# Performance work log

Measured on AMD Instinct MI355X. Metric: run time of the kernel, lower is better.

Reference implementation:

```python
import jax, jax.numpy as jnp
import numpy as np

D_MODEL = 1024
N_HEADS = 16
HEAD_DIM = D_MODEL // N_HEADS
SCALE = HEAD_DIM ** -0.5
MIN_VAL = jnp.finfo(jnp.float32).min


def setup_inputs() -> dict:
    key = jax.random.key(0)
    ks = jax.random.split(key, 7)
    B, T = 1, 2048
    s = D_MODEL ** -0.5
    return {
        "x": jax.random.normal(ks[0], (B, T, D_MODEL), dtype=jnp.float32),
        "Wq": jax.random.normal(ks[1], (D_MODEL, D_MODEL), dtype=jnp.float32) * s,
        "Wk1": jax.random.normal(ks[2], (D_MODEL, D_MODEL), dtype=jnp.float32) * s,
        "Wk2": jax.random.normal(ks[3], (D_MODEL, D_MODEL), dtype=jnp.float32) * s,
        "Wv": jax.random.normal(ks[4], (D_MODEL, D_MODEL), dtype=jnp.float32) * s,
        "Wo": jax.random.normal(ks[5], (D_MODEL, D_MODEL), dtype=jnp.float32) * s,
        "lambda_logit": jnp.zeros((N_HEADS,), dtype=jnp.float32),  # logit(0.5)=0
    }


def _split_heads(y):
    B, T, _ = y.shape
    return y.reshape(B, T, N_HEADS, HEAD_DIM).transpose(0, 2, 1, 3)  # [B,H,T,hd]


def reference(x, Wq, Wk1, Wk2, Wv, Wo, lambda_logit):
    B, T, _ = x.shape
    q = _split_heads(x @ Wq.T)
    k1 = _split_heads(x @ Wk1.T)
    k2 = _split_heads(x @ Wk2.T)
    v = _split_heads(x @ Wv.T)

    s1 = jnp.einsum("bhqd,bhkd->bhqk", q, k1) * SCALE
    s2 = jnp.einsum("bhqd,bhkd->bhqk", q, k2) * SCALE

    causal = jnp.arange(T)[None, :] <= jnp.arange(T)[:, None]  # [T,T] keep mask
    s1 = jnp.where(causal[None, None], s1, MIN_VAL)
    s2 = jnp.where(causal[None, None], s2, MIN_VAL)

    attn_exp = jax.nn.softmax(s1, axis=-1)
    attn_noise = jax.nn.softmax(s2, axis=-1)
    lam = jax.nn.sigmoid(lambda_logit)[None, :, None, None]
    attn = attn_exp - lam * attn_noise
    denom = jnp.maximum(jnp.sum(jnp.abs(attn), axis=-1, keepdims=True), 1e-6)
    attn = attn / denom

    out = jnp.einsum("bhqk,bhkd->bhqd", attn, v)
    out = out.transpose(0, 2, 1, 3).reshape(B, T, D_MODEL)
    return out @ Wo.T
```

## Files before the change

### kernel.cpp

```cpp
#include <hip/hip_runtime.h>

#define T_SEQ 2048
#define DM 1024
#define NH 16
#define HD 64
#define SC2 0.1803368801111731f
#define LS 80

typedef unsigned short u16;
typedef unsigned int u32;
typedef __attribute__((ext_vector_type(8))) short bf16x8;
typedef __attribute__((ext_vector_type(4))) float f32x4;

static __device__ __forceinline__ f32x4 mfma16(bf16x8 a, bf16x8 b, f32x4 c) {
    return __builtin_amdgcn_mfma_f32_16x16x32_bf16(a, b, c, 0, 0, 0);
}
static __device__ __forceinline__ float bf2f(u16 u) {
    union { u32 i; float f; } v; v.i = ((u32)u) << 16; return v.f;
}
static __device__ __forceinline__ u16 f2bf(float f) {
    union { float f; u32 i; } v; v.f = f;
    u32 x = v.i;
    x += 0x7FFFu + ((x >> 16) & 1u);
    return (u16)(x >> 16);
}
static __device__ __forceinline__ u32 pk2(float lo, float hi) {
    return (u32)f2bf(lo) | ((u32)f2bf(hi) << 16);
}
static __device__ __forceinline__ uint4 ld8(const void* src, size_t idx, int f) {
    if (f) return *(const uint4*)((const u16*)src + idx);
    const float* s = (const float*)src + idx;
    uint4 a = *(const uint4*)s;
    uint4 b = *(const uint4*)(s + 4);
    const float* af = (const float*)&a;
    const float* bf = (const float*)&b;
    uint4 r;
    r.x = pk2(af[0], af[1]); r.y = pk2(af[2], af[3]);
    r.z = pk2(bf[0], bf[1]); r.w = pk2(bf[2], bf[3]);
    return r;
}
static __device__ __forceinline__ float qsum16(float v) {
#pragma unroll
    for (int o = 1; o < 16; o <<= 1) v += __shfl_xor(v, o, 64);
    return v;
}
static __device__ __forceinline__ float ex2(float x) {
    return __builtin_amdgcn_exp2f(x);
}

static __device__ __forceinline__ void gl16(const u16* g, u16* l) {
    __builtin_amdgcn_global_load_lds(
        (const __attribute__((address_space(1))) void*)g,
        (__attribute__((address_space(3))) void*)l,
        16, 0, 0);
}

template <int NISS>
static __device__ __forceinline__ void stage_async(const u16* src, size_t row0,
                                                   size_t lds_, size_t col0,
                                                   u16* dst, int tid) {
#pragma unroll
    for (int it = 0; it < NISS; it++) {
        int r = it * 32 + (tid >> 3);
        int cg = (tid & 7) ^ (r & 7);
        gl16(&src[(row0 + r) * lds_ + col0 + cg * 8], &dst[(it * 256 + tid) * 8]);
    }
}
template <int NISS>
static __device__ __forceinline__ void stage_sync(const void* src, size_t row0,
                                                  size_t lds_, size_t col0,
                                                  u16* dst, int tid, int f) {
#pragma unroll
    for (int it = 0; it < NISS; it++) {
        int r = it * 32 + (tid >> 3);
        int cg = (tid & 7) ^ (r & 7);
        *(uint4*)(&dst[(it * 256 + tid) * 8]) =
            ld8(src, (row0 + r) * lds_ + col0 + cg * 8, f);
    }
}
static __device__ __forceinline__ bf16x8 frag(const u16* buf, int R, int co) {
    return *(const bf16x8*)(&buf[R * 64 + co]);
}

__global__ void detect_lam(const u16* __restrict__ x, const void* __restrict__ lamsrc,
                           int* __restrict__ flag, float* __restrict__ lamf) {
    __shared__ int tot;
    if (threadIdx.x == 0) tot = 0;
    __syncthreads();
    int c = 0;
    for (int i = threadIdx.x; i < 1024; i += 256) {
        u16 v = x[2 * i];
        int e = (v >> 7) & 0xFF;
        c += (e >= 110 && e <= 140) ? 1 : 0;
    }
    atomicAdd(&tot, c);
    __syncthreads();
    const int f = (tot >= 512) ? 1 : 0;
    if (threadIdx.x == 0) *flag = f;
    if (threadIdx.x < NH) {
        float v = f ? bf2f(((const u16*)lamsrc)[threadIdx.x])
                    : ((const float*)lamsrc)[threadIdx.x];
        lamf[threadIdx.x] = 1.0f / (1.0f + __expf(-v));
    }
}

__global__ __launch_bounds__(256) void qkv_gemm(
    const void* __restrict__ xs, const void* __restrict__ wq,
    const void* __restrict__ wk1, const void* __restrict__ wk2,
    const void* __restrict__ wv, const int* __restrict__ flag,
    u16* __restrict__ qd, u16* __restrict__ k1d, u16* __restrict__ k2d,
    u16* __restrict__ vtd) {
    __shared__ __align__(16) u16 As[2][128 * 64];
    __shared__ __align__(16) u16 Bs[2][64 * 64];

    const int f = *flag;
    const int w = blockIdx.x >> 4;
    const int n0 = (blockIdx.x & 15) * 64;
    const int m0 = blockIdx.y * 128;
    const void* Bpv = (w == 0) ? wq : (w == 1) ? wk1 : (w == 2) ? wk2 : wv;
    const u16* xb = (const u16*)xs;
    const u16* Bb = (const u16*)Bpv;

    const int tid = threadIdx.x;
    const int lane = tid & 63, wave = tid >> 6;
    const int lr = lane & 15, quad = lane >> 4;
    const int wm = (wave >> 1) * 64, wn = (wave & 1) * 32;
    const int sw = lr & 7;

    f32x4 acc[4][2];
#pragma unroll
    for (int i = 0; i < 4; i++)
#pragma unroll
        for (int j = 0; j < 2; j++) acc[i][j] = (f32x4){0.f, 0.f, 0.f, 0.f};

    if (f) {
        stage_async<4>(xb, m0, DM, 0, As[0], tid);
        stage_async<2>(Bb, n0, DM, 0, Bs[0], tid);
    }
    for (int k0 = 0; k0 < DM; k0 += 64) {
        const int cur = (k0 >> 6) & 1;
        __syncthreads();
        if (f) {
            if (k0 + 64 < DM) {
                stage_async<4>(xb, m0, DM, k0 + 64, As[cur ^ 1], tid);
                stage_async<2>(Bb, n0, DM, k0 + 64, Bs[cur ^ 1], tid);
            }
        } else {
            stage_sync<4>(xs, m0, DM, k0, As[cur], tid, 0);
            stage_sync<2>(Bpv, n0, DM, k0, Bs[cur], tid, 0);
            __syncthreads();
        }
#pragma unroll
        for (int kk = 0; kk < 2; kk++) {
            const int co = ((kk * 4 + quad) ^ sw) * 8;
            bf16x8 af[4], bfr[2];
#pragma unroll
            for (int i = 0; i < 4; i++) af[i] = frag(As[cur], wm + i * 16 + lr, co);
#pragma unroll
            for (int j = 0; j < 2; j++) bfr[j] = frag(Bs[cur], wn + j * 16 + lr, co);
#pragma unroll
            for (int i = 0; i < 4; i++)
#pragma unroll
                for (int j = 0; j < 2; j++) acc[i][j] = mfma16(af[i], bfr[j], acc[i][j]);
        }
    }

#pragma unroll
    for (int i = 0; i < 4; i++)
#pragma unroll
        for (int j = 0; j < 2; j++)
#pragma unroll
            for (int r = 0; r < 4; r++) {
                int t = m0 + wm + i * 16 + quad * 4 + r;
                int o = n0 + wn + j * 16 + lr;
                u16 vbits = f2bf(acc[i][j][r]);
                int hh = o >> 6, d0 = o & 63;
                if (w == 3)
                    vtd[((size_t)hh * HD + d0) * T_SEQ + t] = vbits;
                else
                    ((w == 0) ? qd : (w == 1) ? k1d : k2d)[((size_t)hh * T_SEQ + t) * HD + d0] = vbits;
            }
}

__global__ __launch_bounds__(256) void attn_kernel(
    const u16* __restrict__ qg, const u16* __restrict__ k1g,
    const u16* __restrict__ k2g, const u16* __restrict__ vtg,
    const float* __restrict__ lamf, u16* __restrict__ ao) {
    __shared__ __align__(16) u16 k1s[2][64 * 64];
    __shared__ __align__(16) u16 k2s[2][64 * 64];
    __shared__ __align__(16) u16 vs[2][64 * 64];
    __shared__ __align__(16) u16 ps[4][16 * LS];

    const int b = blockIdx.x;
    const int h = b & 15;
    const int bi = b >> 4;
    const int qt = (bi < 16) ? bi : 47 - bi;
    const int t0 = qt * 64;
    const int tid = threadIdx.x;
    const int lane = tid & 63, wave = tid >> 6;
    const int lr = lane & 15, quad = lane >> 4;
    const int wm = wave * 16;
    const float lam = lamf[h];
    const int sw = lr & 7;

    const u16* qh = qg + (size_t)h * T_SEQ * HD;
    const u16* k1h = k1g + (size_t)h * T_SEQ * HD;
    const u16* k2h = k2g + (size_t)h * T_SEQ * HD;
    const u16* vh = vtg + (size_t)h * HD * T_SEQ;

    bf16x8 aq[2];
#pragma unroll
    for (int kk = 0; kk < 2; kk++)
        aq[kk] = *(const bf16x8*)(&qh[(size_t)(t0 + wm + lr) * HD + kk * 32 + quad * 8]);

    const int nkt = qt + 1;

    stage_async<2>(k1h, 0, HD, 0, k1s[0], tid);
    stage_async<2>(k2h, 0, HD, 0, k2s[0], tid);

    float z1a[4] = {0.f, 0.f, 0.f, 0.f}, z2a[4] = {0.f, 0.f, 0.f, 0.f};

    for (int kt = 0; kt < nkt; kt++) {
        const int cur = kt & 1;
        __syncthreads();
        if (kt + 1 < nkt) {
            stage_async<2>(k1h, (size_t)(kt + 1) * 64, HD, 0, k1s[cur ^ 1], tid);
            stage_async<2>(k2h, (size_t)(kt + 1) * 64, HD, 0, k2s[cur ^ 1], tid);
        }

        f32x4 sa[4], sb[4];
#pragma unroll
        for (int j = 0; j < 4; j++) { sa[j] = (f32x4){0.f,0.f,0.f,0.f}; sb[j] = (f32x4){0.f,0.f,0.f,0.f}; }
#pragma unroll
        for (int kk = 0; kk < 2; kk++) {
            const int co = ((kk * 4 + quad) ^ sw) * 8;
#pragma unroll
            for (int j = 0; j < 4; j++) {
                bf16x8 b1 = frag(k1s[cur], j * 16 + lr, co);
                bf16x8 b2 = frag(k2s[cur], j * 16 + lr, co);
                sa[j] = mfma16(aq[kk], b1, sa[j]);
                sb[j] = mfma16(aq[kk], b2, sb[j]);
            }
        }

        if (kt < qt) {
#pragma unroll
            for (int r = 0; r < 4; r++)
#pragma unroll
                for (int j = 0; j < 4; j++) {
                    z1a[r] += ex2(sa[j][r] * SC2);
                    z2a[r] += ex2(sb[j][r] * SC2);
                }
        } else {
#pragma unroll
            for (int r = 0; r < 4; r++) {
                const int grow = t0 + wm + quad * 4 + r;
#pragma unroll
                for (int j = 0; j < 4; j++) {
                    int gcol = kt * 64 + j * 16 + lr;
                    if (gcol <= grow) {
                        z1a[r] += ex2(sa[j][r] * SC2);
                        z2a[r] += ex2(sb[j][r] * SC2);
                    }
                }
            }
        }
    }

    float z1i[4], z2i[4];
#pragma unroll
    for (int r = 0; r < 4; r++) {
        z1i[r] = 1.f / qsum16(z1a[r]);
        z2i[r] = lam / qsum16(z2a[r]);
    }

    f32x4 oac[4];
#pragma unroll
    for (int j = 0; j < 4; j++) oac[j] = (f32x4){0.f, 0.f, 0.f, 0.f};
    float dacc[4] = {0.f, 0.f, 0.f, 0.f};

    __syncthreads();
    stage_async<2>(k1h, 0, HD, 0, k1s[0], tid);
    stage_async<2>(k2h, 0, HD, 0, k2s[0], tid);
    stage_async<2>(vh, 0, T_SEQ, 0, vs[0], tid);

    for (int kt = 0; kt < nkt; kt++) {
        const int cur = kt & 1;
        __syncthreads();
        if (kt + 1 < nkt) {
            stage_async<2>(k1h, (size_t)(kt + 1) * 64, HD, 0, k1s[cur ^ 1], tid);
            stage_async<2>(k2h, (size_t)(kt + 1) * 64, HD, 0, k2s[cur ^ 1], tid);
            stage_async<2>(vh, 0, T_SEQ, (size_t)(kt + 1) * 64, vs[cur ^ 1], tid);
        }

        f32x4 sa[4], sb[4];
#pragma unroll
        for (int j = 0; j < 4; j++) { sa[j] = (f32x4){0.f,0.f,0.f,0.f}; sb[j] = (f32x4){0.f,0.f,0.f,0.f}; }
#pragma unroll
        for (int kk = 0; kk < 2; kk++) {
            const int co = ((kk * 4 + quad) ^ sw) * 8;
#pragma unroll
            for (int j = 0; j < 4; j++) {
                bf16x8 b1 = frag(k1s[cur], j * 16 + lr, co);
                bf16x8 b2 = frag(k2s[cur], j * 16 + lr, co);
                sa[j] = mfma16(aq[kk], b1, sa[j]);
                sb[j] = mfma16(aq[kk], b2, sb[j]);
            }
        }

        if (kt < qt) {
#pragma unroll
            for (int r = 0; r < 4; r++)
#pragma unroll
                for (int j = 0; j < 4; j++) {
                    float p = ex2(sa[j][r] * SC2) * z1i[r] - ex2(sb[j][r] * SC2) * z2i[r];
                    dacc[r] += fabsf(p);
                    ps[wave][(quad * 4 + r) * LS + j * 16 + lr] = f2bf(p);
                }
        } else {
#pragma unroll
            for (int r = 0; r < 4; r++) {
                const int grow = t0 + wm + quad * 4 + r;
#pragma unroll
                for (int j = 0; j < 4; j++) {
                    int gcol = kt * 64 + j * 16 + lr;
                    float p = 0.f;
                    if (gcol <= grow)
                        p = ex2(sa[j][r] * SC2) * z1i[r] - ex2(sb[j][r] * SC2) * z2i[r];
                    dacc[r] += fabsf(p);
                    ps[wave][(quad * 4 + r) * LS + j * 16 + lr] = f2bf(p);
                }
            }
        }

#pragma unroll
        for (int kk = 0; kk < 2; kk++) {
            bf16x8 pa = *(const bf16x8*)(&ps[wave][lr * LS + kk * 32 + quad * 8]);
            const int co = ((kk * 4 + quad) ^ sw) * 8;
#pragma unroll
            for (int j = 0; j < 4; j++) {
                bf16x8 vb = frag(vs[cur], j * 16 + lr, co);
                oac[j] = mfma16(pa, vb, oac[j]);
            }
        }
    }

    float dnm[4];
#pragma unroll
    for (int r = 0; r < 4; r++) dnm[r] = 1.f / fmaxf(qsum16(dacc[r]), 1e-6f);
#pragma unroll
    for (int j = 0; j < 4; j++)
#pragma unroll
        for (int r = 0; r < 4; r++) {
            int rowl = wm + quad * 4 + r;
            float val = oac[j][r] * dnm[r];
            ao[(size_t)(t0 + rowl) * DM + h * HD + j * 16 + lr] = f2bf(val);
        }
}

__global__ __launch_bounds__(256) void out_gemm(
    const u16* __restrict__ ab, const void* __restrict__ wo,
    const int* __restrict__ flag, void* __restrict__ outp) {
    __shared__ __align__(16) u16 As[2][128 * 64];
    __shared__ __align__(16) u16 Bs[2][64 * 64];

    const int f = *flag;
    const int n0 = blockIdx.x * 64;
    const int m0 = blockIdx.y * 128;
    const u16* wb = (const u16*)wo;
    const int tid = threadIdx.x;
    const int lane = tid & 63, wave = tid >> 6;
    const int lr = lane & 15, quad = lane >> 4;
    const int wm = (wave >> 1) * 64, wn = (wave & 1) * 32;
    const int sw = lr & 7;

    f32x4 acc[4][2];
#pragma unroll
    for (int i = 0; i < 4; i++)
#pragma unroll
        for (int j = 0; j < 2; j++) acc[i][j] = (f32x4){0.f, 0.f, 0.f, 0.f};

    if (f) {
        stage_async<4>(ab, m0, DM, 0, As[0], tid);
        stage_async<2>(wb, n0, DM, 0, Bs[0], tid);
    }
    for (int k0 = 0; k0 < DM; k0 += 64) {
        const int cur = (k0 >> 6) & 1;
        __syncthreads();
        if (f) {
            if (k0 + 64 < DM) {
                stage_async<4>(ab, m0, DM, k0 + 64, As[cur ^ 1], tid);
                stage_async<2>(wb, n0, DM, k0 + 64, Bs[cur ^ 1], tid);
            }
        } else {
            stage_sync<4>(ab, m0, DM, k0, As[cur], tid, 1);
            stage_sync<2>(wo, n0, DM, k0, Bs[cur], tid, 0);
            __syncthreads();
        }
#pragma unroll
        for (int kk = 0; kk < 2; kk++) {
            const int co = ((kk * 4 + quad) ^ sw) * 8;
            bf16x8 af[4], bfr[2];
#pragma unroll
            for (int i = 0; i < 4; i++) af[i] = frag(As[cur], wm + i * 16 + lr, co);
#pragma unroll
            for (int j = 0; j < 2; j++) bfr[j] = frag(Bs[cur], wn + j * 16 + lr, co);
#pragma unroll
            for (int i = 0; i < 4; i++)
#pragma unroll
                for (int j = 0; j < 2; j++) acc[i][j] = mfma16(af[i], bfr[j], acc[i][j]);
        }
    }

#pragma unroll
    for (int i = 0; i < 4; i++)
#pragma unroll
        for (int j = 0; j < 2; j++)
#pragma unroll
            for (int r = 0; r < 4; r++) {
                int t = m0 + wm + i * 16 + quad * 4 + r;
                int o = n0 + wn + j * 16 + lr;
                float val = acc[i][j][r];
                if (f)
                    ((u16*)outp)[(size_t)t * DM + o] = f2bf(val);
                else
                    ((float*)outp)[(size_t)t * DM + o] = val;
            }
}

extern "C" void kernel_launch(void* const* d_in, const int* in_sizes, int n_in,
                              void* d_out, int out_size, void* d_ws, size_t ws_size,
                              hipStream_t stream) {
    char* ws = (char*)d_ws;
    int* flag = (int*)(ws + 0);
    float* lamf = (float*)(ws + 256);
    u16* qd  = (u16*)(ws + ((size_t)16 << 20));
    u16* k1d = (u16*)(ws + ((size_t)20 << 20));
    u16* k2d = (u16*)(ws + ((size_t)24 << 20));
    u16* vtd = (u16*)(ws + ((size_t)28 << 20));
    u16* ao  = (u16*)(ws + ((size_t)32 << 20));

    detect_lam<<<1, 256, 0, stream>>>((const u16*)d_in[0], d_in[6], flag, lamf);
    qkv_gemm<<<dim3(64, 16), 256, 0, stream>>>(d_in[0], d_in[1], d_in[2], d_in[3],
                                               d_in[4], flag, qd, k1d, k2d, vtd);
    attn_kernel<<<dim3(512), 256, 0, stream>>>(qd, k1d, k2d, vtd, lamf, ao);
    out_gemm<<<dim3(16, 16), 256, 0, stream>>>(ao, d_in[5], flag, d_out);
}
```

Before: 231.4 us.

## Split attention into two-pass kernels with key-tile parity split and normalize pass

Replaces the single two-pass attention kernel with separate normalizer and output kernels. Each launches 1024 blocks that handle alternating key tiles by parity, and a new kernel combines the partial outputs and the |attn| denominators. The query scale is folded into the Q projection epilogue, and P is converted to bf16 by truncation instead of rounding. This doubles parallelism to better fill the GPU, at the cost of losing double-buffered async staging, writing bf16 partial outputs to global memory, and launching two extra kernels.

```diff
diff --git a/kernel.cpp b/kernel.cpp
--- a/kernel.cpp
+++ b/kernel.cpp
@@ -23,6 +23,10 @@
     u32 x = v.i;
     x += 0x7FFFu + ((x >> 16) & 1u);
     return (u16)(x >> 16);
+}
+static __device__ __forceinline__ u16 f2bf_t(float f) {
+    union { float f; u32 i; } v; v.f = f;
+    return (u16)(v.i >> 16);
 }
 static __device__ __forceinline__ u32 pk2(float lo, float hi) {
     return (u32)f2bf(lo) | ((u32)f2bf(hi) << 16);
@@ -173,7 +177,9 @@
             for (int r = 0; r < 4; r++) {
                 int t = m0 + wm + i * 16 + quad * 4 + r;
                 int o = n0 + wn + j * 16 + lr;
-                u16 vbits = f2bf(acc[i][j][r]);
+                float val = acc[i][j][r];
+                if (w == 0) val *= SC2;
+                u16 vbits = f2bf(val);
                 int hh = o >> 6, d0 = o & 63;
                 if (w == 3)
                     vtd[((size_t)hh * HD + d0) * T_SEQ + t] = vbits;
@@ -182,26 +188,104 @@
             }
 }
 
-__global__ __launch_bounds__(256) void attn_kernel(
+#define ATTN_MAP()                                            \
+    const int b = blockIdx.x;                                 \
+    const int par = b >> 9;                                   \
+    const int rem = b & 511;                                  \
+    const int h = rem & 15;                                   \
+    const int bi = rem >> 4;                                  \
+    const int qt = (bi < 16) ? bi : 47 - bi;                  \
+    const int t0 = qt * 64;                                   \
+    const int tid = threadIdx.x;                              \
+    const int lane = tid & 63, wave = tid >> 6;               \
+    const int lr = lane & 15, quad = lane >> 4;               \
+    const int wm = wave * 16;                                 \
+    const int sw = lr & 7;
+
+__global__ __launch_bounds__(256) void attn_a(
+    const u16* __restrict__ qg, const u16* __restrict__ k1g,
+    const u16* __restrict__ k2g, float* __restrict__ zp) {
+    __shared__ __align__(16) u16 k1s[64 * 64];
+    __shared__ __align__(16) u16 k2s[64 * 64];
+    ATTN_MAP();
+
+    const u16* qh = qg + (size_t)h * T_SEQ * HD;
+    const u16* k1h = k1g + (size_t)h * T_SEQ * HD;
+    const u16* k2h = k2g + (size_t)h * T_SEQ * HD;
+
+    bf16x8 aq[2];
+#pragma unroll
+    for (int kk = 0; kk < 2; kk++)
+        aq[kk] = *(const bf16x8*)(&qh[(size_t)(t0 + wm + lr) * HD + kk * 32 + quad * 8]);
+
+    float z1a[4] = {0.f, 0.f, 0.f, 0.f}, z2a[4] = {0.f, 0.f, 0.f, 0.f};
+
+    for (int kt = par; kt <= qt; kt += 2) {
+        __syncthreads();
+        stage_async<2>(k1h, (size_t)kt * 64, HD, 0, k1s, tid);
+        stage_async<2>(k2h, (size_t)kt * 64, HD, 0, k2s, tid);
+        __syncthreads();
+
+        f32x4 sa[4], sb[4];
+#pragma unroll
+        for (int j = 0; j < 4; j++) { sa[j] = (f32x4){0.f,0.f,0.f,0.f}; sb[j] = (f32x4){0.f,0.f,0.f,0.f}; }
+#pragma unroll
+        for (int kk = 0; kk < 2; kk++) {
+            const int co = ((kk * 4 + quad) ^ sw) * 8;
+#pragma unroll
+            for (int j = 0; j < 4; j++) {
+                sa[j] = mfma16(aq[kk], frag(k1s, j * 16 + lr, co), sa[j]);
+                sb[j] = mfma16(aq[kk], frag(k2s, j * 16 + lr, co), sb[j]);
+            }
+        }
+
+        if (kt < qt) {
+#pragma unroll
+            for (int r = 0; r < 4; r++)
+#pragma unroll
+                for (int j = 0; j < 4; j++) {
+                    z1a[r] += ex2(sa[j][r]);
+                    z2a[r] += ex2(sb[j][r]);
+                }
+        } else {
+#pragma unroll
+            for (int r = 0; r < 4; r++) {
+                const int grow = t0 + wm + quad * 4 + r;
+#pragma unroll
+                for (int j = 0; j < 4; j++) {
+                    int gcol = kt * 64 + j * 16 + lr;
+                    if (gcol <= grow) {
+                        z1a[r] += ex2(sa[j][r]);
+                        z2a[r] += ex2(sb[j][r]);
+                    }
+                }
+            }
+        }
+    }
+
+#pragma unroll
+    for (int r = 0; r < 4; r++) {
+        float s1 = qsum16(z1a[r]);
+        float s2 = qsum16(z2a[r]);
+        if (lr == 0) {
+            int row = t0 + wm + quad * 4 + r;
+            zp[((size_t)(par * 2 + 0) * NH + h) * T_SEQ + row] = s1;
+            zp[((size_t)(par * 2 + 1) * NH + h) * T_SEQ + row] = s2;
+        }
+    }
+}
+
+__global__ __launch_bounds__(256) void attn_b(
     const u16* __restrict__ qg, const u16* __restrict__ k1g,
     const u16* __restrict__ k2g, const u16* __restrict__ vtg,
-    const float* __restrict__ lamf, u16* __restrict__ ao) {
-    __shared__ __align__(16) u16 k1s[2][64 * 64];
-    __shared__ __align__(16) u16 k2s[2][64 * 64];
-    __shared__ __align__(16) u16 vs[2][64 * 64];
+    const float* __restrict__ zp, const float* __restrict__ lamf,
+    float* __restrict__ dpart, u16* __restrict__ opart) {
+    __shared__ __align__(16) u16 k1s[64 * 64];
+    __shared__ __align__(16) u16 k2s[64 * 64];
+    __shared__ __align__(16) u16 vs[64 * 64];
     __shared__ __align__(16) u16 ps[4][16 * LS];
-
-    const int b = blockIdx.x;
-    const int h = b & 15;
-    const int bi = b >> 4;
-    const int qt = (bi < 16) ? bi : 47 - bi;
-    const int t0 = qt * 64;
-    const int tid = threadIdx.x;
-    const int lane = tid & 63, wave = tid >> 6;
-    const int lr = lane & 15, quad = lane >> 4;
-    const int wm = wave * 16;
+    ATTN_MAP();
     const float lam = lamf[h];
-    const int sw = lr & 7;
 
     const u16* qh = qg + (size_t)h * T_SEQ * HD;
     const u16* k1h = k1g + (size_t)h * T_SEQ * HD;
@@ -213,20 +297,27 @@
     for (int kk = 0; kk < 2; kk++)
         aq[kk] = *(const bf16x8*)(&qh[(size_t)(t0 + wm + lr) * HD + kk * 32 + quad * 8]);
 
-    const int nkt = qt + 1;
-
-    stage_async<2>(k1h, 0, HD, 0, k1s[0], tid);
-    stage_async<2>(k2h, 0, HD, 0, k2s[0], tid);
-
-    float z1a[4] = {0.f, 0.f, 0.f, 0.f}, z2a[4] = {0.f, 0.f, 0.f, 0.f};
-
-    for (int kt = 0; kt < nkt; kt++) {
-        const int cur = kt & 1;
+    float z1i[4], z2i[4];
+#pragma unroll
+    for (int r = 0; r < 4; r++) {
+        int row = t0 + wm + quad * 4 + r;
+        float z1 = zp[((size_t)0 * NH + h) * T_SEQ + row] + zp[((size_t)2 * NH + h) * T_SEQ + row];
+        float z2 = zp[((size_t)1 * NH + h) * T_SEQ + row] + zp[((size_t)3 * NH + h) * T_SEQ + row];
+        z1i[r] = 1.f / z1;
+        z2i[r] = lam / z2;
+    }
+
+    f32x4 oac[4];
+#pragma unroll
+    for (int j = 0; j < 4; j++) oac[j] = (f32x4){0.f, 0.f, 0.f, 0.f};
+    float dacc[4] = {0.f, 0.f, 0.f, 0.f};
+
+    for (int kt = par; kt <= qt; kt += 2) {
         __syncthreads();
-        if (kt + 1 < nkt) {
-            stage_async<2>(k1h, (size_t)(kt + 1) * 64, HD, 0, k1s[cur ^ 1], tid);
-            stage_async<2>(k2h, (size_t)(kt + 1) * 64, HD, 0, k2s[cur ^ 1], tid);
-        }
+        stage_async<2>(k1h, (size_t)kt * 64, HD, 0, k1s, tid);
+        stage_async<2>(k2h, (size_t)kt * 64, HD, 0, k2s, tid);
+        stage_async<2>(vh, 0, T_SEQ, (size_t)kt * 64, vs, tid);
+        __syncthreads();
 
         f32x4 sa[4], sb[4];
 #pragma unroll
@@ -236,10 +327,8 @@
             const int co = ((kk * 4 + quad) ^ sw) * 8;
 #pragma unroll
             for (int j = 0; j < 4; j++) {
-                bf16x8 b1 = frag(k1s[cur], j * 16 + lr, co);
-                bf16x8 b2 = frag(k2s[cur], j * 16 + lr, co);
-                sa[j] = mfma16(aq[kk], b1, sa[j]);
-                sb[j] = mfma16(aq[kk], b2, sb[j]);
+                sa[j] = mfma16(aq[kk], frag(k1s, j * 16 + lr, co), sa[j]);
+                sb[j] = mfma16(aq[kk], frag(k2s, j * 16 + lr, co), sb[j]);
             }
         }
 
@@ -248,74 +337,9 @@
             for (int r = 0; r < 4; r++)
 #pragma unroll
                 for (int j = 0; j < 4; j++) {
-                    z1a[r] += ex2(sa[j][r] * SC2);
-                    z2a[r] += ex2(sb[j][r] * SC2);
-                }
-        } else {
-#pragma unroll
-            for (int r = 0; r < 4; r++) {
-                const int grow = t0 + wm + quad * 4 + r;
-#pragma unroll
-                for (int j = 0; j < 4; j++) {
-                    int gcol = kt * 64 + j * 16 + lr;
-                    if (gcol <= grow) {
-                        z1a[r] += ex2(sa[j][r] * SC2);
-                        z2a[r] += ex2(sb[j][r] * SC2);
-                    }
-                }
-            }
-        }
-    }
-
-    float z1i[4], z2i[4];
-#pragma unroll
-    for (int r = 0; r < 4; r++) {
-        z1i[r] = 1.f / qsum16(z1a[r]);
-        z2i[r] = lam / qsum16(z2a[r]);
-    }
-
-    f32x4 oac[4];
-#pragma unroll
-    for (int j = 0; j < 4; j++) oac[j] = (f32x4){0.f, 0.f, 0.f, 0.f};
-    float dacc[4] = {0.f, 0.f, 0.f, 0.f};
-
-    __syncthreads();
-    stage_async<2>(k1h, 0, HD, 0, k1s[0], tid);
-    stage_async<2>(k2h, 0, HD, 0, k2s[0], tid);
-    stage_async<2>(vh, 0, T_SEQ, 0, vs[0], tid);
-
-    for (int kt = 0; kt < nkt; kt++) {
-        const int cur = kt & 1;
-        __syncthreads();
-        if (kt + 1 < nkt) {
-            stage_async<2>(k1h, (size_t)(kt + 1) * 64, HD, 0, k1s[cur ^ 1], tid);
-            stage_async<2>(k2h, (size_t)(kt + 1) * 64, HD, 0, k2s[cur ^ 1], tid);
-            stage_async<2>(vh, 0, T_SEQ, (size_t)(kt + 1) * 64, vs[cur ^ 1], tid);
-        }
-
-        f32x4 sa[4], sb[4];
-#pragma unroll
-        for (int j = 0; j < 4; j++) { sa[j] = (f32x4){0.f,0.f,0.f,0.f}; sb[j] = (f32x4){0.f,0.f,0.f,0.f}; }
-#pragma unroll
-        for (int kk = 0; kk < 2; kk++) {
-            const int co = ((kk * 4 + quad) ^ sw) * 8;
-#pragma unroll
-            for (int j = 0; j < 4; j++) {
-                bf16x8 b1 = frag(k1s[cur], j * 16 + lr, co);
-                bf16x8 b2 = frag(k2s[cur], j * 16 + lr, co);
-                sa[j] = mfma16(aq[kk], b1, sa[j]);
-                sb[j] = mfma16(aq[kk], b2, sb[j]);
-            }
-        }
-
-        if (kt < qt) {
-#pragma unroll
-            for (int r = 0; r < 4; r++)
-#pragma unroll
-                for (int j = 0; j < 4; j++) {
-                    float p = ex2(sa[j][r] * SC2) * z1i[r] - ex2(sb[j][r] * SC2) * z2i[r];
+                    float p = ex2(sa[j][r]) * z1i[r] - ex2(sb[j][r]) * z2i[r];
                     dacc[r] += fabsf(p);
-                    ps[wave][(quad * 4 + r) * LS + j * 16 + lr] = f2bf(p);
+                    ps[wave][(quad * 4 + r) * LS + j * 16 + lr] = f2bf_t(p);
                 }
         } else {
 #pragma unroll
@@ -326,9 +350,9 @@
                     int gcol = kt * 64 + j * 16 + lr;
                     float p = 0.f;
                     if (gcol <= grow)
-                        p = ex2(sa[j][r] * SC2) * z1i[r] - ex2(sb[j][r] * SC2) * z2i[r];
+                        p = ex2(sa[j][r]) * z1i[r] - ex2(sb[j][r]) * z2i[r];
                     dacc[r] += fabsf(p);
-                    ps[wave][(quad * 4 + r) * LS + j * 16 + lr] = f2bf(p);
+                    ps[wave][(quad * 4 + r) * LS + j * 16 + lr] = f2bf_t(p);
                 }
             }
         }
@@ -338,24 +362,52 @@
             bf16x8 pa = *(const bf16x8*)(&ps[wave][lr * LS + kk * 32 + quad * 8]);
             const int co = ((kk * 4 + quad) ^ sw) * 8;
 #pragma unroll
-            for (int j = 0; j < 4; j++) {
-                bf16x8 vb = frag(vs[cur], j * 16 + lr, co);
-                oac[j] = mfma16(pa, vb, oac[j]);
-            }
-        }
-    }
-
-    float dnm[4];
-#pragma unroll
-    for (int r = 0; r < 4; r++) dnm[r] = 1.f / fmaxf(qsum16(dacc[r]), 1e-6f);
+            for (int j = 0; j < 4; j++)
+                oac[j] = mfma16(pa, frag(vs, j * 16 + lr, co), oac[j]);
+        }
+    }
+
+#pragma unroll
+    for (int r = 0; r < 4; r++) {
+        float ds = qsum16(dacc[r]);
+        if (lr == 0) {
+            int row = t0 + wm + quad * 4 + r;
+            dpart[((size_t)par * NH + h) * T_SEQ + row] = ds;
+        }
+    }
 #pragma unroll
     for (int j = 0; j < 4; j++)
 #pragma unroll
         for (int r = 0; r < 4; r++) {
-            int rowl = wm + quad * 4 + r;
-            float val = oac[j][r] * dnm[r];
-            ao[(size_t)(t0 + rowl) * DM + h * HD + j * 16 + lr] = f2bf(val);
-        }
+            int row = t0 + wm + quad * 4 + r;
+            opart[(size_t)par * T_SEQ * DM + (size_t)row * DM + h * HD + j * 16 + lr] =
+                f2bf(oac[j][r]);
+        }
+}
+
+__global__ __launch_bounds__(256) void normalize_o(
+    const u16* __restrict__ opart, const float* __restrict__ dpart,
+    u16* __restrict__ ao) {
+    int g = blockIdx.x * 256 + threadIdx.x;
+    int t = g >> 7;
+    int cc = g & 127;
+    int d0 = cc * 8;
+    int h = d0 >> 6;
+    float dsum = dpart[(size_t)h * T_SEQ + t] + dpart[(size_t)(NH + h) * T_SEQ + t];
+    float rs = 1.f / fmaxf(dsum, 1e-6f);
+    uint4 a = *(const uint4*)(&opart[(size_t)t * DM + d0]);
+    uint4 bqq = *(const uint4*)(&opart[(size_t)T_SEQ * DM + (size_t)t * DM + d0]);
+    const u32* au = (const u32*)&a;
+    const u32* bu = (const u32*)&bqq;
+    uint4 out;
+    u32* ou = (u32*)&out;
+#pragma unroll
+    for (int i = 0; i < 4; i++) {
+        float lo = (bf2f((u16)(au[i] & 0xFFFF)) + bf2f((u16)(bu[i] & 0xFFFF))) * rs;
+        float hi = (bf2f((u16)(au[i] >> 16)) + bf2f((u16)(bu[i] >> 16))) * rs;
+        ou[i] = pk2(lo, hi);
+    }
+    *(uint4*)(&ao[(size_t)t * DM + d0]) = out;
 }
 
 __global__ __launch_bounds__(256) void out_gemm(
@@ -434,15 +486,20 @@
     char* ws = (char*)d_ws;
     int* flag = (int*)(ws + 0);
     float* lamf = (float*)(ws + 256);
+    float* zp    = (float*)(ws + ((size_t)1 << 20));
+    float* dpart = (float*)(ws + ((size_t)2 << 20));
     u16* qd  = (u16*)(ws + ((size_t)16 << 20));
     u16* k1d = (u16*)(ws + ((size_t)20 << 20));
     u16* k2d = (u16*)(ws + ((size_t)24 << 20));
     u16* vtd = (u16*)(ws + ((size_t)28 << 20));
     u16* ao  = (u16*)(ws + ((size_t)32 << 20));
+    u16* opart = (u16*)(ws + ((size_t)36 << 20));
 
     detect_lam<<<1, 256, 0, stream>>>((const u16*)d_in[0], d_in[6], flag, lamf);
     qkv_gemm<<<dim3(64, 16), 256, 0, stream>>>(d_in[0], d_in[1], d_in[2], d_in[3],
                                                d_in[4], flag, qd, k1d, k2d, vtd);
-    attn_kernel<<<dim3(512), 256, 0, stream>>>(qd, k1d, k2d, vtd, lamf, ao);
+    attn_a<<<dim3(1024), 256, 0, stream>>>(qd, k1d, k2d, zp);
+    attn_b<<<dim3(1024), 256, 0, stream>>>(qd, k1d, k2d, vtd, zp, lamf, dpart, opart);
+    normalize_o<<<dim3(1024), 256, 0, stream>>>(opart, dpart, ao);
     out_gemm<<<dim3(16, 16), 256, 0, stream>>>(ao, d_in[5], flag, d_out);
 }
```

Measured after the change: 225.0 us. 2.7% less time.
